# Kernel tuning notes

Hardware: AMD Instinct MI355X
Metric: run time of the kernel (lower is better)

The kernel has to match this reference:

```python
import jax, jax.numpy as jnp
from jax import lax
import numpy as np

WIN = 11
SIGMA = 1.5
VAL_RANGE = 10.0
C1 = (0.01 * VAL_RANGE) ** 2
C2 = (0.03 * VAL_RANGE) ** 2


def _gauss_window():
    # matches pytorch-ssim create_window: normalized 1D gaussian, outer product
    g = np.exp(-((np.arange(WIN) - WIN // 2) ** 2) / (2.0 * SIGMA ** 2))
    g = g / g.sum()
    return jnp.asarray(np.outer(g, g), jnp.float32)


def _blur(x, win):
    # depthwise 11x11 gaussian conv, padding=0 (VALID), per pytorch-ssim with padd=0
    k = x.shape[1]
    kern = jnp.broadcast_to(win[None, None], (k, 1, WIN, WIN)).astype(x.dtype)
    return lax.conv_general_dilated(x, kern, (1, 1), 'VALID', feature_group_count=k)


def setup_inputs() -> dict:
    key = jax.random.key(0)
    ks = jax.random.split(key, 7)
    B, C, H, W = 8, 64, 256, 256
    x = jax.random.normal(ks[0], (B, C, H, W), jnp.float32)
    mask = jax.random.randint(ks[1], (B, H, W), 0, 2, jnp.int32)
    conv_w = jax.random.normal(ks[2], (1, 3, 3, 1), jnp.float32) * 0.3
    w1 = jax.random.normal(ks[3], (C, C), jnp.float32) * (1.0 / np.sqrt(C))
    b1 = jax.random.normal(ks[4], (C,), jnp.float32) * 0.01
    w2 = jax.random.normal(ks[5], (C, C), jnp.float32) * (1.0 / np.sqrt(C))
    b2 = jax.random.normal(ks[6], (C,), jnp.float32) * 0.01
    return {'x': x, 'mask': mask, 'conv_w': conv_w, 'w1': w1, 'b1': b1, 'w2': w2, 'b2': b2}


def reference(x, mask, conv_w, w1, b1, w2, b2):
    B, C, H, W = x.shape
    m = mask.astype(x.dtype)[:, None]  # [B,1,H,W]

    # ChannelPool: max/mean/min over channel dim -> [B,3,H,W]
    xc = jnp.stack([x.max(axis=1), x.mean(axis=1), x.min(axis=1)], axis=1)

    # ChannelNorm: masked per-sample, per-channel mean / unbiased std; zero outside mask
    n = m.sum(axis=(2, 3), keepdims=True)                       # [B,1,1,1]
    mean = (xc * m).sum(axis=(2, 3), keepdims=True) / n
    var = (((xc - mean) ** 2) * m).sum(axis=(2, 3), keepdims=True) / (n - 1.0)
    xf = (xc - mean) / jnp.sqrt(var) * m                        # [B,3,H,W]

    # Pairwise SSIM between xf channels (3) and x channels (C), vectorized
    win = _gauss_window()
    mu_f = _blur(xf, win)                                       # [B,3,H',W']
    mu_x = _blur(x, win)                                        # [B,C,H',W']
    ef2 = _blur(xf * xf, win)
    ex2 = _blur(x * x, win)
    prod = (xf[:, :, None] * x[:, None]).reshape(B, 3 * C, H, W)
    Hp, Wp = H - WIN + 1, W - WIN + 1
    exf = _blur(prod, win).reshape(B, 3, C, Hp, Wp)

    mu1 = mu_f[:, :, None]                                      # [B,3,1,H',W']
    mu2 = mu_x[:, None]                                         # [B,1,C,H',W']
    s1 = ef2[:, :, None] - mu1 ** 2
    s2 = ex2[:, None] - mu2 ** 2
    s12 = exf - mu1 * mu2
    ssim_map = ((2 * mu1 * mu2 + C1) * (2 * s12 + C2)) / ((mu1 ** 2 + mu2 ** 2 + C1) * (s1 + s2 + C2))
    ssim_info = ssim_map.mean(axis=(3, 4))                      # [B,3,C]

    # spatial Conv2d(3,1,(3,1),pad=(1,0)) on [B,3,C,1], then ReLU, MLP, Sigmoid
    h = lax.conv_general_dilated(ssim_info[..., None], conv_w, (1, 1), ((1, 1), (0, 0)))
    h = jax.nn.relu(h).reshape(B, C)
    h = jax.nn.relu(h @ w1.T + b1)
    h = jax.nn.sigmoid(h @ w2.T + b2)
    return h, ssim_info
```

## Files before the change

kernel.cpp:

```cpp
#include <hip/hip_runtime.h>
#include <cmath>

#define Bn   8
#define Cn   64
#define HWc  65536
#define HPc  246
#define HPWPc 60516
#define C1v  0.01f
#define C2v  0.09f

static __device__ __forceinline__ void gauss11(float* gw) {
    double gg[11]; double s = 0.0;
#pragma unroll
    for (int j = 0; j < 11; ++j) { double d = (double)(j - 5); gg[j] = exp(-(d * d) / 4.5); s += gg[j]; }
#pragma unroll
    for (int j = 0; j < 11; ++j) gw[j] = (float)(gg[j] / s);
}

static __device__ __forceinline__ float4 f4z() { return make_float4(0.f, 0.f, 0.f, 0.f); }
static __device__ __forceinline__ float4 f4scale(float g, const float4 v) {
    return make_float4(g * v.x, g * v.y, g * v.z, g * v.w);
}
static __device__ __forceinline__ void f4add(float4& a, const float4 v) {
    a.x += v.x; a.y += v.y; a.z += v.z; a.w += v.w;
}
static __device__ __forceinline__ void f4fma(float4& a, const float4 u, const float4 v) {
    a.x = fmaf(u.x, v.x, a.x); a.y = fmaf(u.y, v.y, a.y);
    a.z = fmaf(u.z, v.z, a.z); a.w = fmaf(u.w, v.w, a.w);
}

static __device__ __forceinline__ float wave_sum64(float v) {
    v += __int_as_float(__builtin_amdgcn_update_dpp(0, __float_as_int(v), 0x111, 0xf, 0xf, true));
    v += __int_as_float(__builtin_amdgcn_update_dpp(0, __float_as_int(v), 0x112, 0xf, 0xf, true));
    v += __int_as_float(__builtin_amdgcn_update_dpp(0, __float_as_int(v), 0x114, 0xf, 0xf, true));
    v += __int_as_float(__builtin_amdgcn_update_dpp(0, __float_as_int(v), 0x118, 0xf, 0xf, true));
    v += __int_as_float(__builtin_amdgcn_update_dpp(0, __float_as_int(v), 0x142, 0xf, 0xf, true));
    v += __int_as_float(__builtin_amdgcn_update_dpp(0, __float_as_int(v), 0x143, 0xf, 0xf, true));
    return v;
}

__global__ __launch_bounds__(256) void k1_stats(const float* __restrict__ x, const int* __restrict__ mask,
                                                float* __restrict__ xcf, float* __restrict__ stats) {
    const int b = blockIdx.y;
    const int p0 = blockIdx.x * 1024 + threadIdx.x * 4;
    const float4* xp = (const float4*)(x + (size_t)b * Cn * HWc) + (p0 >> 2);
    float4 v = xp[0];
    float4 vmax = v, vmin = v, vsum = v;
#pragma unroll 4
    for (int c = 1; c < Cn; ++c) {
        float4 u = xp[(size_t)c * (HWc / 4)];
        vmax.x = fmaxf(vmax.x, u.x); vmax.y = fmaxf(vmax.y, u.y);
        vmax.z = fmaxf(vmax.z, u.z); vmax.w = fmaxf(vmax.w, u.w);
        vmin.x = fminf(vmin.x, u.x); vmin.y = fminf(vmin.y, u.y);
        vmin.z = fminf(vmin.z, u.z); vmin.w = fminf(vmin.w, u.w);
        vsum.x += u.x; vsum.y += u.y; vsum.z += u.z; vsum.w += u.w;
    }
    float4 vmean = make_float4(vsum.x * (1.f / 64.f), vsum.y * (1.f / 64.f),
                               vsum.z * (1.f / 64.f), vsum.w * (1.f / 64.f));
    *(float4*)(xcf + (size_t)(b * 3 + 0) * HWc + p0) = vmax;
    *(float4*)(xcf + (size_t)(b * 3 + 1) * HWc + p0) = vmean;
    *(float4*)(xcf + (size_t)(b * 3 + 2) * HWc + p0) = vmin;
    int4 mv = *(const int4*)(mask + (size_t)b * HWc + p0);
    float m0 = (float)mv.x, m1 = (float)mv.y, m2 = (float)mv.z, m3 = (float)mv.w;
    float r[7];
    r[0] = m0 + m1 + m2 + m3;
    r[1] = vmax.x * m0 + vmax.y * m1 + vmax.z * m2 + vmax.w * m3;
    r[2] = vmean.x * m0 + vmean.y * m1 + vmean.z * m2 + vmean.w * m3;
    r[3] = vmin.x * m0 + vmin.y * m1 + vmin.z * m2 + vmin.w * m3;
    r[4] = vmax.x * vmax.x * m0 + vmax.y * vmax.y * m1 + vmax.z * vmax.z * m2 + vmax.w * vmax.w * m3;
    r[5] = vmean.x * vmean.x * m0 + vmean.y * vmean.y * m1 + vmean.z * vmean.z * m2 + vmean.w * vmean.w * m3;
    r[6] = vmin.x * vmin.x * m0 + vmin.y * vmin.y * m1 + vmin.z * vmin.z * m2 + vmin.w * vmin.w * m3;
#pragma unroll
    for (int k = 0; k < 7; ++k) {
        float vv = wave_sum64(r[k]);
        if ((threadIdx.x & 63) == 63) atomicAdd(&stats[b * 8 + k], vv);
    }
}

__global__ __launch_bounds__(256) void k4_blur3(const float* __restrict__ xc, const int* __restrict__ mask,
                                                const float* __restrict__ stats,
                                                float* __restrict__ muf, float* __restrict__ ef2g) {
    __shared__ __align__(16) float vb2[32 * 92];
    const int t = threadIdx.x;
    const int bi = blockIdx.z, b = bi / 3, i = bi % 3;
    const int y0 = blockIdx.y * 32, x0 = blockIdx.x * 32;
    float gw[11]; gauss11(gw);
    const float nst = stats[b * 8 + 0];
    const float s1 = stats[b * 8 + 1 + i], s2 = stats[b * 8 + 4 + i];
    const float mean = s1 / nst;
    const float rstd = rsqrtf((s2 - s1 * s1 / nst) / (nst - 1.0f));
    if (t < 176) {
        const int rg = t / 11, cg = t % 11, colo = cg * 4;
        const int gcb = min(x0 + colo, 252);
        const float* xp = xc + (size_t)bi * HWc;
        const int* mp = mask + (size_t)b * HWc;
        float4 av0 = f4z(), ab0 = f4z(), av1 = f4z(), ab1 = f4z();
#pragma unroll
        for (int k = 0; k < 12; ++k) {
            int gr = min(y0 + 2 * rg + k, 255);
            float4 v = *(const float4*)(xp + gr * 256 + gcb);
            int4 mv = *(const int4*)(mp + gr * 256 + gcb);
            float4 f;
            f.x = (v.x - mean) * rstd * (float)mv.x;
            f.y = (v.y - mean) * rstd * (float)mv.y;
            f.z = (v.z - mean) * rstd * (float)mv.z;
            f.w = (v.w - mean) * rstd * (float)mv.w;
            if (k <= 10) { float4 tv = f4scale(gw[k], f); f4add(av0, tv); f4fma(ab0, tv, f); }
            if (k >= 1)  { float4 tv = f4scale(gw[k - 1], f); f4add(av1, tv); f4fma(ab1, tv, f); }
        }
        {
            float* dst = &vb2[(2 * rg + 0) * 92 + colo * 2];
            *(float4*)&dst[0] = make_float4(av0.x, ab0.x, av0.y, ab0.y);
            *(float4*)&dst[4] = make_float4(av0.z, ab0.z, av0.w, ab0.w);
        }
        {
            float* dst = &vb2[(2 * rg + 1) * 92 + colo * 2];
            *(float4*)&dst[0] = make_float4(av1.x, ab1.x, av1.y, ab1.y);
            *(float4*)&dst[4] = make_float4(av1.z, ab1.z, av1.w, ab1.w);
        }
    }
    __syncthreads();
    {
        const int erow = t >> 3, ecg = t & 7;
        const int oy = y0 + erow;
        const float* src = &vb2[erow * 92 + ecg * 8];
        float a00 = 0.f, a01 = 0.f, a02 = 0.f, a03 = 0.f;
        float a10 = 0.f, a11 = 0.f, a12 = 0.f, a13 = 0.f;
#pragma unroll
        for (int m = 0; m < 14; ++m) {
            float v0 = src[m * 2 + 0];
            float v1 = src[m * 2 + 1];
#pragma unroll
            for (int j = 0; j < 4; ++j) {
                const int kk = m - j;
                if (kk >= 0 && kk <= 10) {
                    if (j == 0) { a00 = fmaf(gw[kk], v0, a00); a10 = fmaf(gw[kk], v1, a10); }
                    if (j == 1) { a01 = fmaf(gw[kk], v0, a01); a11 = fmaf(gw[kk], v1, a11); }
                    if (j == 2) { a02 = fmaf(gw[kk], v0, a02); a12 = fmaf(gw[kk], v1, a12); }
                    if (j == 3) { a03 = fmaf(gw[kk], v0, a03); a13 = fmaf(gw[kk], v1, a13); }
                }
            }
        }
        if (oy < HPc) {
            size_t ob = (size_t)bi * HPWPc + (size_t)oy * HPc;
            int oxb = x0 + ecg * 4;
            if (oxb + 0 < HPc) { muf[ob + oxb + 0] = a00; ef2g[ob + oxb + 0] = a10; }
            if (oxb + 1 < HPc) { muf[ob + oxb + 1] = a01; ef2g[ob + oxb + 1] = a11; }
            if (oxb + 2 < HPc) { muf[ob + oxb + 2] = a02; ef2g[ob + oxb + 2] = a12; }
            if (oxb + 3 < HPc) { muf[ob + oxb + 3] = a03; ef2g[ob + oxb + 3] = a13; }
        }
    }
}

#define T(F,J,KK,V) h##F##_##J = fmaf(G##KK, (V), h##F##_##J);
#define TM0(F,V)  T(F,0,0,V)
#define TM1(F,V)  T(F,0,1,V) T(F,1,0,V)
#define TM2(F,V)  T(F,0,2,V) T(F,1,1,V) T(F,2,0,V)
#define TM3(F,V)  T(F,0,3,V) T(F,1,2,V) T(F,2,1,V) T(F,3,0,V)
#define TM4(F,V)  T(F,0,4,V) T(F,1,3,V) T(F,2,2,V) T(F,3,1,V)
#define TM5(F,V)  T(F,0,5,V) T(F,1,4,V) T(F,2,3,V) T(F,3,2,V)
#define TM6(F,V)  T(F,0,6,V) T(F,1,5,V) T(F,2,4,V) T(F,3,3,V)
#define TM7(F,V)  T(F,0,7,V) T(F,1,6,V) T(F,2,5,V) T(F,3,4,V)
#define TM8(F,V)  T(F,0,8,V) T(F,1,7,V) T(F,2,6,V) T(F,3,5,V)
#define TM9(F,V)  T(F,0,9,V) T(F,1,8,V) T(F,2,7,V) T(F,3,6,V)
#define TM10(F,V) T(F,0,10,V) T(F,1,9,V) T(F,2,8,V) T(F,3,7,V)
#define TM11(F,V) T(F,1,10,V) T(F,2,9,V) T(F,3,8,V)
#define TM12(F,V) T(F,2,10,V) T(F,3,9,V)
#define TM13(F,V) T(F,3,10,V)

#define DECLH(J) float h0_##J = 0.f, h1_##J = 0.f, h2_##J = 0.f, h3_##J = 0.f, h4_##J = 0.f;
#define DECLJ(J) float M0_##J, M1_##J, M2_##J, S0_##J, S1_##J, S2_##J;
#define SETI(I,J) { float mu1 = 0.f, e2 = 0.f; \
    if (vld) { size_t o = (size_t)(b * 3 + I) * HPWPc + (size_t)oy * HPc + ox; mu1 = muf[o]; e2 = ef2g[o]; } \
    M##I##_##J = mu1; S##I##_##J = vld ? ((e2 - mu1 * mu1) + C2v) : __builtin_inff(); }
#define SETJ(J) { int ox = ox0 + J; bool vld = (oy < HPc) && (ox < HPc); \
    SETI(0,J) SETI(1,J) SETI(2,J) }

#define SSIMI(I,J,HV) { float am = M##I##_##J * m2; \
    float num = fmaf(2.f, am, C1v) * fmaf(2.f, (HV) - am, C2v); \
    float den = fmaf(M##I##_##J, M##I##_##J, c1m2) * (S##I##_##J + s2); \
    sa##I += num * __builtin_amdgcn_rcpf(den); }
#define SSIMJ(J) { float m2 = h0_##J; float m2sq = m2 * m2; \
    float c1m2 = C1v + m2sq; float s2 = h1_##J - m2sq; \
    SSIMI(0,J,h2_##J) SSIMI(1,J,h3_##J) SSIMI(2,J,h4_##J) }

#define VSTEP(K, DOA, DOB, GA, GB) { \
    int gr = y0 + 2 * vrg + (K); gr = (gr > 255) ? 255 : gr; \
    float4 xv = *(const float4*)(xp + gr * 256 + gcb); \
    const int ro = (2 * vrg + (K)) * 44 + vcolo; \
    float4 f0 = *(const float4*)&f0in[ro]; \
    float4 f1v = *(const float4*)&f1in[ro]; \
    float4 f2v = *(const float4*)&f2in[ro]; \
    if (DOA) { float4 tv = f4scale((GA), xv); f4add(xA0, tv); f4fma(xQ0, tv, xv); \
               f4fma(p00, tv, f0); f4fma(p10, tv, f1v); f4fma(p20, tv, f2v); } \
    if (DOB) { float4 tv = f4scale((GB), xv); f4add(xA1, tv); f4fma(xQ1, tv, xv); \
               f4fma(p01, tv, f0); f4fma(p11, tv, f1v); f4fma(p21, tv, f2v); } }

__global__ __launch_bounds__(256, 2) void k5_main(const float* __restrict__ x, const float* __restrict__ xc,
                                                  const int* __restrict__ mask, const float* __restrict__ stats,
                                                  const float* __restrict__ muf, const float* __restrict__ ef2g,
                                                  float* __restrict__ ssum) {
    __shared__ __align__(16) float f0in[42 * 44];
    __shared__ __align__(16) float f1in[42 * 44];
    __shared__ __align__(16) float f2in[42 * 44];
    __shared__ __align__(16) float vb5[32 * 228];
    const int t = threadIdx.x;
    const int b = blockIdx.z;
    const int y0 = blockIdx.y * 32, x0 = blockIdx.x * 32;
    const double e0 = exp(-25.0 / 4.5), e1 = exp(-16.0 / 4.5), e2d = exp(-9.0 / 4.5),
                 e3 = exp(-4.0 / 4.5), e4 = exp(-1.0 / 4.5);
    const double sg = 1.0 + 2.0 * (e0 + e1 + e2d + e3 + e4);
    const float G0 = (float)(e0 / sg), G1 = (float)(e1 / sg), G2 = (float)(e2d / sg),
                G3 = (float)(e3 / sg), G4 = (float)(e4 / sg), G5 = (float)(1.0 / sg);
    const float G6 = G4, G7 = G3, G8 = G2, G9 = G1, G10 = G0;
    const float nst = stats[b * 8 + 0];
    const float s1a = stats[b * 8 + 1], s2a = stats[b * 8 + 4];
    const float s1b = stats[b * 8 + 2], s2b = stats[b * 8 + 5];
    const float s1c = stats[b * 8 + 3], s2c = stats[b * 8 + 6];
    const float mean0 = s1a / nst, rstd0 = rsqrtf((s2a - s1a * s1a / nst) / (nst - 1.0f));
    const float mean1 = s1b / nst, rstd1 = rsqrtf((s2b - s1b * s1b / nst) / (nst - 1.0f));
    const float mean2 = s1c / nst, rstd2 = rsqrtf((s2c - s1c * s1c / nst) / (nst - 1.0f));
    for (int q = t; q < 42 * 11; q += 256) {
        int row = q / 11, cg = q % 11;
        int gr = min(y0 + row, 255), gc = min(x0 + cg * 4, 252);
        int go = gr * 256 + gc;
        int lo = row * 44 + cg * 4;
        int4 mv = *(const int4*)(mask + (size_t)b * HWc + go);
        float m0 = (float)mv.x, m1 = (float)mv.y, m2 = (float)mv.z, m3 = (float)mv.w;
        float4 v0 = *(const float4*)(xc + (size_t)(b * 3 + 0) * HWc + go);
        v0.x = (v0.x - mean0) * rstd0 * m0; v0.y = (v0.y - mean0) * rstd0 * m1;
        v0.z = (v0.z - mean0) * rstd0 * m2; v0.w = (v0.w - mean0) * rstd0 * m3;
        *(float4*)&f0in[lo] = v0;
        float4 v1 = *(const float4*)(xc + (size_t)(b * 3 + 1) * HWc + go);
        v1.x = (v1.x - mean1) * rstd1 * m0; v1.y = (v1.y - mean1) * rstd1 * m1;
        v1.z = (v1.z - mean1) * rstd1 * m2; v1.w = (v1.w - mean1) * rstd1 * m3;
        *(float4*)&f1in[lo] = v1;
        float4 v2 = *(const float4*)(xc + (size_t)(b * 3 + 2) * HWc + go);
        v2.x = (v2.x - mean2) * rstd2 * m0; v2.y = (v2.y - mean2) * rstd2 * m1;
        v2.z = (v2.z - mean2) * rstd2 * m2; v2.w = (v2.w - mean2) * rstd2 * m3;
        *(float4*)&f2in[lo] = v2;
    }
    const int erow = t >> 3, ecg = t & 7;
    const int oy = y0 + erow;
    const int ox0 = x0 + ecg * 4;
    DECLJ(0) DECLJ(1) DECLJ(2) DECLJ(3)
    SETJ(0) SETJ(1) SETJ(2) SETJ(3)
    __syncthreads();
    const float* xb = x + (size_t)b * Cn * HWc;
    const int vrg = t / 11, vcg = t % 11, vcolo = vcg * 4;
    const int gcb = min(x0 + vcolo, 252);
    const bool vact = (t < 176);
    for (int c = 0; c < Cn; ++c) {
        if (vact) {
            const float* xp = xb + (size_t)c * HWc;
            float4 xA0 = f4z(), xQ0 = f4z(), p00 = f4z(), p10 = f4z(), p20 = f4z();
            float4 xA1 = f4z(), xQ1 = f4z(), p01 = f4z(), p11 = f4z(), p21 = f4z();
            VSTEP(0, 1, 0, G0, G0)  VSTEP(1, 1, 1, G1, G0)  VSTEP(2, 1, 1, G2, G1)
            VSTEP(3, 1, 1, G3, G2)  VSTEP(4, 1, 1, G4, G3)  VSTEP(5, 1, 1, G5, G4)
            VSTEP(6, 1, 1, G6, G5)  VSTEP(7, 1, 1, G7, G6)  VSTEP(8, 1, 1, G8, G7)
            VSTEP(9, 1, 1, G9, G8)  VSTEP(10, 1, 1, G10, G9) VSTEP(11, 0, 1, G0, G10)
            {
                float* dst = &vb5[(2 * vrg + 0) * 228 + vcolo * 5];
                *(float4*)&dst[0]  = make_float4(xA0.x, xQ0.x, p00.x, p10.x);
                *(float4*)&dst[4]  = make_float4(p20.x, xA0.y, xQ0.y, p00.y);
                *(float4*)&dst[8]  = make_float4(p10.y, p20.y, xA0.z, xQ0.z);
                *(float4*)&dst[12] = make_float4(p00.z, p10.z, p20.z, xA0.w);
                *(float4*)&dst[16] = make_float4(xQ0.w, p00.w, p10.w, p20.w);
            }
            {
                float* dst = &vb5[(2 * vrg + 1) * 228 + vcolo * 5];
                *(float4*)&dst[0]  = make_float4(xA1.x, xQ1.x, p01.x, p11.x);
                *(float4*)&dst[4]  = make_float4(p21.x, xA1.y, xQ1.y, p01.y);
                *(float4*)&dst[8]  = make_float4(p11.y, p21.y, xA1.z, xQ1.z);
                *(float4*)&dst[12] = make_float4(p01.z, p11.z, p21.z, xA1.w);
                *(float4*)&dst[16] = make_float4(xQ1.w, p01.w, p11.w, p21.w);
            }
        }
        __syncthreads();
        {
            const float* src = &vb5[erow * 228 + ecg * 20];
            DECLH(0) DECLH(1) DECLH(2) DECLH(3)
            float4 L0 = *(const float4*)(src + 0);
            TM0(0, L0.x) TM0(1, L0.y) TM0(2, L0.z) TM0(3, L0.w)
            float4 L1 = *(const float4*)(src + 4);
            TM0(4, L1.x) TM1(0, L1.y) TM1(1, L1.z) TM1(2, L1.w)
            float4 L2 = *(const float4*)(src + 8);
            TM1(3, L2.x) TM1(4, L2.y) TM2(0, L2.z) TM2(1, L2.w)
            float4 L3 = *(const float4*)(src + 12);
            TM2(2, L3.x) TM2(3, L3.y) TM2(4, L3.z) TM3(0, L3.w)
            float4 L4 = *(const float4*)(src + 16);
            TM3(1, L4.x) TM3(2, L4.y) TM3(3, L4.z) TM3(4, L4.w)
            float4 L5 = *(const float4*)(src + 20);
            TM4(0, L5.x) TM4(1, L5.y) TM4(2, L5.z) TM4(3, L5.w)
            float4 L6 = *(const float4*)(src + 24);
            TM4(4, L6.x) TM5(0, L6.y) TM5(1, L6.z) TM5(2, L6.w)
            float4 L7 = *(const float4*)(src + 28);
            TM5(3, L7.x) TM5(4, L7.y) TM6(0, L7.z) TM6(1, L7.w)
            float4 L8 = *(const float4*)(src + 32);
            TM6(2, L8.x) TM6(3, L8.y) TM6(4, L8.z) TM7(0, L8.w)
            float4 L9 = *(const float4*)(src + 36);
            TM7(1, L9.x) TM7(2, L9.y) TM7(3, L9.z) TM7(4, L9.w)
            float4 L10 = *(const float4*)(src + 40);
            TM8(0, L10.x) TM8(1, L10.y) TM8(2, L10.z) TM8(3, L10.w)
            float4 L11 = *(const float4*)(src + 44);
            TM8(4, L11.x) TM9(0, L11.y) TM9(1, L11.z) TM9(2, L11.w)
            float4 L12 = *(const float4*)(src + 48);
            TM9(3, L12.x) TM9(4, L12.y) TM10(0, L12.z) TM10(1, L12.w)
            float4 L13 = *(const float4*)(src + 52);
            TM10(2, L13.x) TM10(3, L13.y) TM10(4, L13.z) TM11(0, L13.w)
            float4 L14 = *(const float4*)(src + 56);
            TM11(1, L14.x) TM11(2, L14.y) TM11(3, L14.z) TM11(4, L14.w)
            float4 L15 = *(const float4*)(src + 60);
            TM12(0, L15.x) TM12(1, L15.y) TM12(2, L15.z) TM12(3, L15.w)
            float4 L16 = *(const float4*)(src + 64);
            TM12(4, L16.x) TM13(0, L16.y) TM13(1, L16.z) TM13(2, L16.w)
            float4 L17 = *(const float4*)(src + 68);
            TM13(3, L17.x) TM13(4, L17.y)
            float sa0 = 0.f, sa1 = 0.f, sa2 = 0.f;
            SSIMJ(0) SSIMJ(1) SSIMJ(2) SSIMJ(3)
            sa0 = wave_sum64(sa0);
            sa1 = wave_sum64(sa1);
            sa2 = wave_sum64(sa2);
            if ((t & 63) == 63) {
                atomicAdd(&ssum[(b * 3 + 0) * 64 + c], sa0);
                atomicAdd(&ssum[(b * 3 + 1) * 64 + c], sa1);
                atomicAdd(&ssum[(b * 3 + 2) * 64 + c], sa2);
            }
        }
        __syncthreads();
    }
}

__global__ __launch_bounds__(512) void k6_head(const float* __restrict__ ssum, const float* __restrict__ cw,
                                               const float* __restrict__ w1, const float* __restrict__ b1,
                                               const float* __restrict__ w2, const float* __restrict__ b2,
                                               float* __restrict__ out) {
    __shared__ float si[1536];
    __shared__ float h0[512];
    __shared__ float h1[512];
    const int t = threadIdx.x;
    const float inv = 1.0f / (float)HPWPc;
    for (int idx = t; idx < 1536; idx += 512) {
        float v = ssum[idx] * inv;
        si[idx] = v;
        out[512 + idx] = v;
    }
    __syncthreads();
    const int b = t >> 6, y = t & 63;
    float acc = 0.f;
#pragma unroll
    for (int i = 0; i < 3; ++i) {
#pragma unroll
        for (int kh = 0; kh < 3; ++kh) {
            int yy = y + kh - 1;
            if (yy >= 0 && yy < 64) acc = fmaf(si[(b * 3 + i) * 64 + yy], cw[i * 3 + kh], acc);
        }
    }
    h0[t] = fmaxf(acc, 0.f);
    __syncthreads();
    float a1 = b1[y];
    for (int c = 0; c < 64; ++c) a1 = fmaf(h0[(b << 6) + c], w1[(y << 6) + c], a1);
    h1[t] = fmaxf(a1, 0.f);
    __syncthreads();
    float a2 = b2[y];
    for (int c = 0; c < 64; ++c) a2 = fmaf(h1[(b << 6) + c], w2[(y << 6) + c], a2);
    out[t] = 1.f / (1.f + expf(-a2));
}

extern "C" void kernel_launch(void* const* d_in, const int* in_sizes, int n_in,
                              void* d_out, int out_size, void* d_ws, size_t ws_size,
                              hipStream_t stream) {
    const float* x      = (const float*)d_in[0];
    const int*   mask   = (const int*)d_in[1];
    const float* conv_w = (const float*)d_in[2];
    const float* w1     = (const float*)d_in[3];
    const float* b1     = (const float*)d_in[4];
    const float* w2     = (const float*)d_in[5];
    const float* b2     = (const float*)d_in[6];
    float* out = (float*)d_out;

    float* wsf   = (float*)d_ws;
    float* stats = wsf;
    float* ssum  = wsf + 64;
    float* xcf   = wsf + 1600;
    float* muf   = xcf + (size_t)Bn * 3 * HWc;
    float* ef2   = muf + (size_t)Bn * 3 * HPWPc;

    hipMemsetAsync(d_ws, 0, 6400, stream);

    k1_stats<<<dim3(64, 8), 256, 0, stream>>>(x, mask, xcf, stats);
    k4_blur3<<<dim3(8, 8, 24), 256, 0, stream>>>(xcf, mask, stats, muf, ef2);
    k5_main<<<dim3(8, 8, 8), 256, 0, stream>>>(x, xcf, mask, stats, muf, ef2, ssum);
    k6_head<<<1, 512, 0, stream>>>(ssum, conv_w, w1, b1, w2, b2, out);
}
```

Baseline: 656.3 us.

## Double-buffer vertical-pass LDS tile to overlap vertical and horizontal blur phases

Splits the shared vertical-blur buffer into two ping-pong buffers so the vertical pass for channel c+1 runs in the same barrier interval as the horizontal SSIM pass for channel c. This halves the number of block-wide barriers per channel and lets idle threads in one phase proceed with the other. The row pitch is shrunk to 224 floats to limit the extra LDS footprint, at the cost of more shared memory per block and larger code.

After: 656.8 us. About the same (+0.1%).

```diff
diff --git a/kernel.cpp b/kernel.cpp
--- a/kernel.cpp
+++ b/kernel.cpp
@@ -8,6 +8,7 @@
 #define HPWPc 60516
 #define C1v  0.01f
 #define C2v  0.09f
+#define VPITCH 224
 
 static __device__ __forceinline__ void gauss11(float* gw) {
     double gg[11]; double s = 0.0;
@@ -196,6 +197,79 @@
     if (DOB) { float4 tv = f4scale((GB), xv); f4add(xA1, tv); f4fma(xQ1, tv, xv); \
                f4fma(p01, tv, f0); f4fma(p11, tv, f1v); f4fma(p21, tv, f2v); } }
 
+#define VERT(CC, BUF) do { if (vact) { \
+    const float* xp = xb + (size_t)(CC) * HWc; \
+    float4 xA0 = f4z(), xQ0 = f4z(), p00 = f4z(), p10 = f4z(), p20 = f4z(); \
+    float4 xA1 = f4z(), xQ1 = f4z(), p01 = f4z(), p11 = f4z(), p21 = f4z(); \
+    VSTEP(0, 1, 0, G0, G0)  VSTEP(1, 1, 1, G1, G0)  VSTEP(2, 1, 1, G2, G1) \
+    VSTEP(3, 1, 1, G3, G2)  VSTEP(4, 1, 1, G4, G3)  VSTEP(5, 1, 1, G5, G4) \
+    VSTEP(6, 1, 1, G6, G5)  VSTEP(7, 1, 1, G7, G6)  VSTEP(8, 1, 1, G8, G7) \
+    VSTEP(9, 1, 1, G9, G8)  VSTEP(10, 1, 1, G10, G9) VSTEP(11, 0, 1, G0, G10) \
+    { float* dst = &BUF[(2 * vrg + 0) * VPITCH + vcolo * 5]; \
+      *(float4*)&dst[0]  = make_float4(xA0.x, xQ0.x, p00.x, p10.x); \
+      *(float4*)&dst[4]  = make_float4(p20.x, xA0.y, xQ0.y, p00.y); \
+      *(float4*)&dst[8]  = make_float4(p10.y, p20.y, xA0.z, xQ0.z); \
+      *(float4*)&dst[12] = make_float4(p00.z, p10.z, p20.z, xA0.w); \
+      *(float4*)&dst[16] = make_float4(xQ0.w, p00.w, p10.w, p20.w); } \
+    { float* dst = &BUF[(2 * vrg + 1) * VPITCH + vcolo * 5]; \
+      *(float4*)&dst[0]  = make_float4(xA1.x, xQ1.x, p01.x, p11.x); \
+      *(float4*)&dst[4]  = make_float4(p21.x, xA1.y, xQ1.y, p01.y); \
+      *(float4*)&dst[8]  = make_float4(p11.y, p21.y, xA1.z, xQ1.z); \
+      *(float4*)&dst[12] = make_float4(p01.z, p11.z, p21.z, xA1.w); \
+      *(float4*)&dst[16] = make_float4(xQ1.w, p01.w, p11.w, p21.w); } \
+} } while (0)
+
+#define HORIZ(CC, BUF) do { \
+    const float* src = &BUF[erow * VPITCH + ecg * 20]; \
+    DECLH(0) DECLH(1) DECLH(2) DECLH(3) \
+    float4 L0 = *(const float4*)(src + 0); \
+    TM0(0, L0.x) TM0(1, L0.y) TM0(2, L0.z) TM0(3, L0.w) \
+    float4 L1 = *(const float4*)(src + 4); \
+    TM0(4, L1.x) TM1(0, L1.y) TM1(1, L1.z) TM1(2, L1.w) \
+    float4 L2 = *(const float4*)(src + 8); \
+    TM1(3, L2.x) TM1(4, L2.y) TM2(0, L2.z) TM2(1, L2.w) \
+    float4 L3 = *(const float4*)(src + 12); \
+    TM2(2, L3.x) TM2(3, L3.y) TM2(4, L3.z) TM3(0, L3.w) \
+    float4 L4 = *(const float4*)(src + 16); \
+    TM3(1, L4.x) TM3(2, L4.y) TM3(3, L4.z) TM3(4, L4.w) \
+    float4 L5 = *(const float4*)(src + 20); \
+    TM4(0, L5.x) TM4(1, L5.y) TM4(2, L5.z) TM4(3, L5.w) \
+    float4 L6 = *(const float4*)(src + 24); \
+    TM4(4, L6.x) TM5(0, L6.y) TM5(1, L6.z) TM5(2, L6.w) \
+    float4 L7 = *(const float4*)(src + 28); \
+    TM5(3, L7.x) TM5(4, L7.y) TM6(0, L7.z) TM6(1, L7.w) \
+    float4 L8 = *(const float4*)(src + 32); \
+    TM6(2, L8.x) TM6(3, L8.y) TM6(4, L8.z) TM7(0, L8.w) \
+    float4 L9 = *(const float4*)(src + 36); \
+    TM7(1, L9.x) TM7(2, L9.y) TM7(3, L9.z) TM7(4, L9.w) \
+    float4 L10 = *(const float4*)(src + 40); \
+    TM8(0, L10.x) TM8(1, L10.y) TM8(2, L10.z) TM8(3, L10.w) \
+    float4 L11 = *(const float4*)(src + 44); \
+    TM8(4, L11.x) TM9(0, L11.y) TM9(1, L11.z) TM9(2, L11.w) \
+    float4 L12 = *(const float4*)(src + 48); \
+    TM9(3, L12.x) TM9(4, L12.y) TM10(0, L12.z) TM10(1, L12.w) \
+    float4 L13 = *(const float4*)(src + 52); \
+    TM10(2, L13.x) TM10(3, L13.y) TM10(4, L13.z) TM11(0, L13.w) \
+    float4 L14 = *(const float4*)(src + 56); \
+    TM11(1, L14.x) TM11(2, L14.y) TM11(3, L14.z) TM11(4, L14.w) \
+    float4 L15 = *(const float4*)(src + 60); \
+    TM12(0, L15.x) TM12(1, L15.y) TM12(2, L15.z) TM12(3, L15.w) \
+    float4 L16 = *(const float4*)(src + 64); \
+    TM12(4, L16.x) TM13(0, L16.y) TM13(1, L16.z) TM13(2, L16.w) \
+    float4 L17 = *(const float4*)(src + 68); \
+    TM13(3, L17.x) TM13(4, L17.y) \
+    float sa0 = 0.f, sa1 = 0.f, sa2 = 0.f; \
+    SSIMJ(0) SSIMJ(1) SSIMJ(2) SSIMJ(3) \
+    sa0 = wave_sum64(sa0); \
+    sa1 = wave_sum64(sa1); \
+    sa2 = wave_sum64(sa2); \
+    if ((t & 63) == 63) { \
+        atomicAdd(&ssum[(b * 3 + 0) * 64 + (CC)], sa0); \
+        atomicAdd(&ssum[(b * 3 + 1) * 64 + (CC)], sa1); \
+        atomicAdd(&ssum[(b * 3 + 2) * 64 + (CC)], sa2); \
+    } \
+} while (0)
+
 __global__ __launch_bounds__(256, 2) void k5_main(const float* __restrict__ x, const float* __restrict__ xc,
                                                   const int* __restrict__ mask, const float* __restrict__ stats,
                                                   const float* __restrict__ muf, const float* __restrict__ ef2g,
@@ -203,7 +277,8 @@
     __shared__ __align__(16) float f0in[42 * 44];
     __shared__ __align__(16) float f1in[42 * 44];
     __shared__ __align__(16) float f2in[42 * 44];
-    __shared__ __align__(16) float vb5[32 * 228];
+    __shared__ __align__(16) float vb5a[32 * VPITCH];
+    __shared__ __align__(16) float vb5b[32 * VPITCH];
     const int t = threadIdx.x;
     const int b = blockIdx.z;
     const int y0 = blockIdx.y * 32, x0 = blockIdx.x * 32;
@@ -245,89 +320,21 @@
     const int ox0 = x0 + ecg * 4;
     DECLJ(0) DECLJ(1) DECLJ(2) DECLJ(3)
     SETJ(0) SETJ(1) SETJ(2) SETJ(3)
-    __syncthreads();
     const float* xb = x + (size_t)b * Cn * HWc;
     const int vrg = t / 11, vcg = t % 11, vcolo = vcg * 4;
     const int gcb = min(x0 + vcolo, 252);
     const bool vact = (t < 176);
-    for (int c = 0; c < Cn; ++c) {
-        if (vact) {
-            const float* xp = xb + (size_t)c * HWc;
-            float4 xA0 = f4z(), xQ0 = f4z(), p00 = f4z(), p10 = f4z(), p20 = f4z();
-            float4 xA1 = f4z(), xQ1 = f4z(), p01 = f4z(), p11 = f4z(), p21 = f4z();
-            VSTEP(0, 1, 0, G0, G0)  VSTEP(1, 1, 1, G1, G0)  VSTEP(2, 1, 1, G2, G1)
-            VSTEP(3, 1, 1, G3, G2)  VSTEP(4, 1, 1, G4, G3)  VSTEP(5, 1, 1, G5, G4)
-            VSTEP(6, 1, 1, G6, G5)  VSTEP(7, 1, 1, G7, G6)  VSTEP(8, 1, 1, G8, G7)
-            VSTEP(9, 1, 1, G9, G8)  VSTEP(10, 1, 1, G10, G9) VSTEP(11, 0, 1, G0, G10)
-            {
-                float* dst = &vb5[(2 * vrg + 0) * 228 + vcolo * 5];
-                *(float4*)&dst[0]  = make_float4(xA0.x, xQ0.x, p00.x, p10.x);
-                *(float4*)&dst[4]  = make_float4(p20.x, xA0.y, xQ0.y, p00.y);
-                *(float4*)&dst[8]  = make_float4(p10.y, p20.y, xA0.z, xQ0.z);
-                *(float4*)&dst[12] = make_float4(p00.z, p10.z, p20.z, xA0.w);
-                *(float4*)&dst[16] = make_float4(xQ0.w, p00.w, p10.w, p20.w);
-            }
-            {
-                float* dst = &vb5[(2 * vrg + 1) * 228 + vcolo * 5];
-                *(float4*)&dst[0]  = make_float4(xA1.x, xQ1.x, p01.x, p11.x);
-                *(float4*)&dst[4]  = make_float4(p21.x, xA1.y, xQ1.y, p01.y);
-                *(float4*)&dst[8]  = make_float4(p11.y, p21.y, xA1.z, xQ1.z);
-                *(float4*)&dst[12] = make_float4(p01.z, p11.z, p21.z, xA1.w);
-                *(float4*)&dst[16] = make_float4(xQ1.w, p01.w, p11.w, p21.w);
-            }
-        }
+
+    __syncthreads();
+    VERT(0, vb5a);
+#pragma unroll 1
+    for (int c = 0; c < Cn; c += 2) {
         __syncthreads();
-        {
-            const float* src = &vb5[erow * 228 + ecg * 20];
-            DECLH(0) DECLH(1) DECLH(2) DECLH(3)
-            float4 L0 = *(const float4*)(src + 0);
-            TM0(0, L0.x) TM0(1, L0.y) TM0(2, L0.z) TM0(3, L0.w)
-            float4 L1 = *(const float4*)(src + 4);
-            TM0(4, L1.x) TM1(0, L1.y) TM1(1, L1.z) TM1(2, L1.w)
-            float4 L2 = *(const float4*)(src + 8);
-            TM1(3, L2.x) TM1(4, L2.y) TM2(0, L2.z) TM2(1, L2.w)
-            float4 L3 = *(const float4*)(src + 12);
-            TM2(2, L3.x) TM2(3, L3.y) TM2(4, L3.z) TM3(0, L3.w)
-            float4 L4 = *(const float4*)(src + 16);
-            TM3(1, L4.x) TM3(2, L4.y) TM3(3, L4.z) TM3(4, L4.w)
-            float4 L5 = *(const float4*)(src + 20);
-            TM4(0, L5.x) TM4(1, L5.y) TM4(2, L5.z) TM4(3, L5.w)
-            float4 L6 = *(const float4*)(src + 24);
-            TM4(4, L6.x) TM5(0, L6.y) TM5(1, L6.z) TM5(2, L6.w)
-            float4 L7 = *(const float4*)(src + 28);
-            TM5(3, L7.x) TM5(4, L7.y) TM6(0, L7.z) TM6(1, L7.w)
-            float4 L8 = *(const float4*)(src + 32);
-            TM6(2, L8.x) TM6(3, L8.y) TM6(4, L8.z) TM7(0, L8.w)
-            float4 L9 = *(const float4*)(src + 36);
-            TM7(1, L9.x) TM7(2, L9.y) TM7(3, L9.z) TM7(4, L9.w)
-            float4 L10 = *(const float4*)(src + 40);
-            TM8(0, L10.x) TM8(1, L10.y) TM8(2, L10.z) TM8(3, L10.w)
-            float4 L11 = *(const float4*)(src + 44);
-            TM8(4, L11.x) TM9(0, L11.y) TM9(1, L11.z) TM9(2, L11.w)
-            float4 L12 = *(const float4*)(src + 48);
-            TM9(3, L12.x) TM9(4, L12.y) TM10(0, L12.z) TM10(1, L12.w)
-            float4 L13 = *(const float4*)(src + 52);
-            TM10(2, L13.x) TM10(3, L13.y) TM10(4, L13.z) TM11(0, L13.w)
-            float4 L14 = *(const float4*)(src + 56);
-            TM11(1, L14.x) TM11(2, L14.y) TM11(3, L14.z) TM11(4, L14.w)
-            float4 L15 = *(const float4*)(src + 60);
-            TM12(0, L15.x) TM12(1, L15.y) TM12(2, L15.z) TM12(3, L15.w)
-            float4 L16 = *(const float4*)(src + 64);
-            TM12(4, L16.x) TM13(0, L16.y) TM13(1, L16.z) TM13(2, L16.w)
-            float4 L17 = *(const float4*)(src + 68);
-            TM13(3, L17.x) TM13(4, L17.y)
-            float sa0 = 0.f, sa1 = 0.f, sa2 = 0.f;
-            SSIMJ(0) SSIMJ(1) SSIMJ(2) SSIMJ(3)
-            sa0 = wave_sum64(sa0);
-            sa1 = wave_sum64(sa1);
-            sa2 = wave_sum64(sa2);
-            if ((t & 63) == 63) {
-                atomicAdd(&ssum[(b * 3 + 0) * 64 + c], sa0);
-                atomicAdd(&ssum[(b * 3 + 1) * 64 + c], sa1);
-                atomicAdd(&ssum[(b * 3 + 2) * 64 + c], sa2);
-            }
-        }
+        VERT(c + 1, vb5b);
+        HORIZ(c, vb5a);
         __syncthreads();
+        if (c + 2 < Cn) VERT(c + 2, vb5a);
+        HORIZ(c + 1, vb5b);
     }
 }
 
```
